# Optimization experiments

Measured on AMD Instinct MI355X. Metric: run time of the kernel, lower is better.

The kernel has to match this reference:

```python
import jax, jax.numpy as jnp
import numpy as np

L, H, DK = 4, 8, 64
NEG = -1e9
PAD = -9999.0


def _ln(z, g, b, eps=1e-6):
    # LayerNormalization: uses unbiased std (torch default) and divides by (std + eps)
    m = jnp.mean(z, axis=-1, keepdims=True)
    s = jnp.std(z, axis=-1, keepdims=True, ddof=1)
    return g * (z - m) / (s + eps) + b


def _mha(q_in, kv_in, w, bw, pw, pb, lnp, mask):
    B, Sq, D = q_in.shape
    q = (q_in @ w[0] + bw[0]).reshape(B, Sq, H, DK).transpose(0, 2, 1, 3)
    k = (kv_in @ w[1] + bw[1]).reshape(B, -1, H, DK).transpose(0, 2, 1, 3)
    v = (kv_in @ w[2] + bw[2]).reshape(B, -1, H, DK).transpose(0, 2, 1, 3)
    scores = jnp.einsum('bhqd,bhkd->bhqk', q, k) * (1.0 / np.sqrt(DK))
    if mask is not None:
        scores = jnp.where(mask[:, None, :, :], NEG, scores)
    attn = jax.nn.softmax(scores, axis=-1)
    ctx = jnp.einsum('bhqk,bhkd->bhqd', attn, v).transpose(0, 2, 1, 3).reshape(B, Sq, H * DK)
    return _ln(q_in + ctx @ pw + pb, lnp[0], lnp[1])


def _ffn(x, w1, b1, w2, b2, lnp):
    # kernel-1 conv1d == pointwise linear; w1:[d_ff,d_model], w2:[d_model,d_ff]
    h = jax.nn.relu(jnp.einsum('bsd,fd->bsf', x, w1) + b1)
    o = jnp.einsum('bsf,df->bsd', h, w2) + b2
    return _ln(x + o, lnp[0], lnp[1])


def _forward(enc_inputs, dec_inputs, emb_w, emb_b, pos_table,
             e_qkv_w, e_qkv_b, e_pw, e_pb, e_ln1, e_w1, e_b1, e_w2, e_b2, e_ln2,
             ds_qkv_w, ds_qkv_b, ds_pw, ds_pb, d_ln1,
             dc_qkv_w, dc_qkv_b, dc_pw, dc_pb, d_ln2,
             d_w1, d_b1, d_w2, d_b2, d_ln3):
    B, Se, F = enc_inputs.shape
    Sd = dec_inputs.shape[1]
    # ConvEmbeddingLayer: kernel-1 conv producing (d_model - n_features) channels, concat with raw inputs
    enc = jnp.concatenate([enc_inputs, jnp.einsum('bsf,of->bso', enc_inputs, emb_w) + emb_b], axis=-1)
    dec = jnp.concatenate([dec_inputs, jnp.einsum('bsf,of->bso', dec_inputs, emb_w) + emb_b], axis=-1)
    # PosEncoding with full lengths -> rows 1..S of the padded table
    enc = enc + pos_table[1:Se + 1]
    dec = dec + pos_table[1:Sd + 1]
    # masks per get_attn_pad_mask / get_attn_subsequent_mask
    enc_pad = jnp.sum(enc_inputs, axis=-1) <= PAD  # [B,Se]
    dec_pad = jnp.sum(dec_inputs, axis=-1) <= PAD  # [B,Sd]
    enc_mask = jnp.broadcast_to(enc_pad[:, None, :], (B, Se, Se))
    causal = jnp.triu(jnp.ones((Sd, Sd), dtype=bool), 1)
    dec_self_mask = jnp.broadcast_to(dec_pad[:, None, :], (B, Sd, Sd)) | causal
    cross_mask = jnp.broadcast_to(enc_pad[:, None, :], (B, Sd, Se))
    for i in range(L):
        enc = _mha(enc, enc, e_qkv_w[i], e_qkv_b[i], e_pw[i], e_pb[i], e_ln1[i], enc_mask)
        enc = _ffn(enc, e_w1[i], e_b1[i], e_w2[i], e_b2[i], e_ln2[i])
    for i in range(L):
        dec = _mha(dec, dec, ds_qkv_w[i], ds_qkv_b[i], ds_pw[i], ds_pb[i], d_ln1[i], dec_self_mask)
        dec = _mha(dec, enc, dc_qkv_w[i], dc_qkv_b[i], dc_pw[i], dc_pb[i], d_ln2[i], cross_mask)
        dec = _ffn(dec, d_w1[i], d_b1[i], d_w2[i], d_b2[i], d_ln3[i])
    return dec


def setup_inputs() -> dict:
    B, Se, Sd, F, Dm, Dff = 8, 512, 512, 32, 512, 2048
    key = jax.random.key(0)
    ks = iter(jax.random.split(key, 32))
    s = 0.02

    def n(shape, sc=s):
        return jax.random.normal(next(ks), shape, jnp.float32) * sc

    # sinusoidal PosEncoding table with leading pad row
    pos = np.arange(Se, dtype=np.float64)[:, None]
    j = np.arange(Dm)[None, :]
    ang = pos / np.power(10000.0, 2.0 * (j // 2) / Dm)
    ang[:, 0::2] = np.sin(ang[:, 0::2])
    ang[:, 1::2] = np.cos(ang[:, 1::2])
    pos_table = jnp.asarray(np.concatenate([np.zeros((1, Dm)), ang]).astype(np.float32))

    ln = jnp.broadcast_to(jnp.stack([jnp.ones(Dm), jnp.zeros(Dm)]), (L, 2, Dm)).astype(jnp.float32) + 0.0
    return {
        'enc_inputs': jax.random.normal(next(ks), (B, Se, F), jnp.float32),
        'dec_inputs': jax.random.normal(next(ks), (B, Sd, F), jnp.float32),
        'emb_w': n((Dm - F, F)), 'emb_b': jnp.zeros(Dm - F, jnp.float32),
        'pos_table': pos_table,
        'e_qkv_w': n((L, 3, Dm, H * DK)), 'e_qkv_b': jnp.zeros((L, 3, H * DK), jnp.float32),
        'e_pw': n((L, H * DK, Dm)), 'e_pb': jnp.zeros((L, Dm), jnp.float32), 'e_ln1': ln,
        'e_w1': n((L, Dff, Dm)), 'e_b1': jnp.zeros((L, Dff), jnp.float32),
        'e_w2': n((L, Dm, Dff)), 'e_b2': jnp.zeros((L, Dm), jnp.float32), 'e_ln2': ln,
        'ds_qkv_w': n((L, 3, Dm, H * DK)), 'ds_qkv_b': jnp.zeros((L, 3, H * DK), jnp.float32),
        'ds_pw': n((L, H * DK, Dm)), 'ds_pb': jnp.zeros((L, Dm), jnp.float32), 'd_ln1': ln,
        'dc_qkv_w': n((L, 3, Dm, H * DK)), 'dc_qkv_b': jnp.zeros((L, 3, H * DK), jnp.float32),
        'dc_pw': n((L, H * DK, Dm)), 'dc_pb': jnp.zeros((L, Dm), jnp.float32), 'd_ln2': ln,
        'd_w1': n((L, Dff, Dm)), 'd_b1': jnp.zeros((L, Dff), jnp.float32),
        'd_w2': n((L, Dm, Dff)), 'd_b2': jnp.zeros((L, Dm), jnp.float32), 'd_ln3': ln,
    }


def reference(enc_inputs, dec_inputs, emb_w, emb_b, pos_table,
              e_qkv_w, e_qkv_b, e_pw, e_pb, e_ln1, e_w1, e_b1, e_w2, e_b2, e_ln2,
              ds_qkv_w, ds_qkv_b, ds_pw, ds_pb, d_ln1,
              dc_qkv_w, dc_qkv_b, dc_pw, dc_pb, d_ln2,
              d_w1, d_b1, d_w2, d_b2, d_ln3):
    return _forward(enc_inputs, dec_inputs, emb_w, emb_b, pos_table,
                    e_qkv_w, e_qkv_b, e_pw, e_pb, e_ln1, e_w1, e_b1, e_w2, e_b2, e_ln2,
                    ds_qkv_w, ds_qkv_b, ds_pw, ds_pb, d_ln1,
                    dc_qkv_w, dc_qkv_b, dc_pw, dc_pb, d_ln2,
                    d_w1, d_b1, d_w2, d_b2, d_ln3)
```

## Files before the change

kernel.cpp:

```cpp
#include <hip/hip_runtime.h>
#include <cstdint>
#include <cstddef>

typedef unsigned short u16;
typedef __bf16 bf16x8 __attribute__((ext_vector_type(8)));
typedef float f32x4 __attribute__((ext_vector_type(4)));

constexpr int Bz = 8, Sq = 512, Hh = 8, DKd = 64, Dm = 512, Dff = 2048, NL = 4;
constexpr int TOK = Bz * Sq;
constexpr size_t MAT = (size_t)512 * 512;
constexpr size_t EL  = (size_t)TOK * Dm;

__device__ __forceinline__ float bf2f(u16 u) {
  union { uint32_t i; float f; } v; v.i = (uint32_t)u << 16; return v.f;
}
__device__ __forceinline__ u16 f2bf(float f) {
  union { float f; uint32_t i; } v; v.f = f;
  uint32_t i = v.i;
  i += 0x7fffu + ((i >> 16) & 1u);
  return (u16)(i >> 16);
}

__device__ __forceinline__ void gload16(const u16* g, u16* l) {
  __builtin_amdgcn_global_load_lds(
      (const __attribute__((address_space(1))) unsigned int*)g,
      (__attribute__((address_space(3))) unsigned int*)l, 16, 0, 0);
}

template<int BM, int BN>
__global__ __launch_bounds__(256)
void gemm_tile(const u16* __restrict__ A, const u16* __restrict__ Bt,
               const float* __restrict__ bias, u16* __restrict__ C,
               int K, int lda, long long sA, int ldb, long long sB,
               int ldc, long long sC, int cmode, int relu, int colofs)
{
  constexpr int HM = BM / 2, HN = BN / 2, MI = HM / 16, NI = HN / 16;
  __shared__ __align__(16) u16 As[BM * 32];
  __shared__ __align__(16) u16 Bs[BN * 32];
  const int bz = blockIdx.z;
  const u16* Ab = A + (size_t)bz * (size_t)sA + (size_t)(blockIdx.y * BM) * lda;
  const u16* Bb = Bt + (size_t)bz * (size_t)sB + (size_t)(blockIdx.x * BN) * ldb;
  const int tid  = threadIdx.x;
  const int lane = tid & 63;
  const int wid  = tid >> 6;
  const int l15  = lane & 15;
  const int quad = lane >> 4;
  const int wm   = wid >> 1, wn = wid & 1;

  f32x4 acc[MI][NI] = {};

  for (int k0 = 0; k0 < K; k0 += 32) {
#pragma unroll
    for (int i = 0; i < BM / 64; ++i) {
      const int s = tid + i * 256;
      const int c = (s & 3) ^ ((s >> 3) & 3);
      gload16(Ab + (size_t)(s >> 2) * lda + k0 + c * 8, As + s * 8);
    }
#pragma unroll
    for (int i = 0; i < BN / 64; ++i) {
      const int s = tid + i * 256;
      const int c = (s & 3) ^ ((s >> 3) & 3);
      gload16(Bb + (size_t)(s >> 2) * ldb + k0 + c * 8, Bs + s * 8);
    }
    __syncthreads();
    bf16x8 af[MI], bfr[NI];
#pragma unroll
    for (int mi = 0; mi < MI; ++mi) {
      const int ra = wm * HM + mi * 16 + l15;
      af[mi] = *(const bf16x8*)(As + ra * 32 + (quad ^ ((ra >> 1) & 3)) * 8);
    }
#pragma unroll
    for (int ni = 0; ni < NI; ++ni) {
      const int rb = wn * HN + ni * 16 + l15;
      bfr[ni] = *(const bf16x8*)(Bs + rb * 32 + (quad ^ ((rb >> 1) & 3)) * 8);
    }
#pragma unroll
    for (int mi = 0; mi < MI; ++mi)
#pragma unroll
      for (int ni = 0; ni < NI; ++ni)
        acc[mi][ni] = __builtin_amdgcn_mfma_f32_16x16x32_bf16(af[mi], bfr[ni], acc[mi][ni], 0, 0, 0);
    __syncthreads();
  }

  const int rblk = blockIdx.y * BM + wm * HM + quad * 4;
  const int cblk = blockIdx.x * BN + wn * HN;
#pragma unroll
  for (int ni = 0; ni < NI; ++ni) {
    const int col  = cblk + ni * 16 + l15;
    const int colx = colofs + col;
    const float bv = bias ? bias[colx] : 0.f;
#pragma unroll
    for (int mi = 0; mi < MI; ++mi) {
#pragma unroll
      for (int r = 0; r < 4; ++r) {
        float v = acc[mi][ni][r] + bv;
        if (relu) v = fmaxf(v, 0.f);
        const int grow = rblk + mi * 16 + r;
        size_t off;
        if (cmode == 0) {
          off = (size_t)bz * (size_t)sC + (size_t)grow * ldc + col;
        } else if (cmode == 3) {
          off = (size_t)(bz >> 3) * 262144 + (size_t)grow * 512 + (size_t)(bz & 7) * 64 + col;
        } else {
          const int sec = colx >> 9, n = colx & 511, h = n >> 6, d = n & 63;
          const int b = grow >> 9, s = grow & 511;
          if (sec == 0) v *= 0.125f;
          if (sec < 2) off = (size_t)sec * EL + (size_t)b * 262144 + (size_t)h * 32768 + (size_t)s * 64 + d;
          else         off = 2 * EL + (size_t)b * 262144 + (size_t)h * 32768 + (size_t)d * 512 + s;
        }
        C[off] = f2bf(v);
      }
    }
  }
}

__global__ __launch_bounds__(256)
void flash_attn(const u16* __restrict__ q, const u16* __restrict__ k,
                const u16* __restrict__ v, const unsigned char* __restrict__ pad,
                u16* __restrict__ ctx, int mtype)
{
  __shared__ __align__(16) u16 KVs[8192];
  __shared__ __align__(16) u16 Pw[4][2048];
  const int bh = blockIdx.y, b = bh >> 3, h = bh & 7;
  const int qt = blockIdx.x;
  const int tid = threadIdx.x, lane = tid & 63, wid = tid >> 6;
  const int l15 = lane & 15, quad = lane >> 4;
  const size_t bho = (size_t)bh * 32768;
  const int qrow = qt * 64 + wid * 16 + l15;
  const int qcd  = qt * 64 + wid * 16 + quad * 4;

  unsigned char* Ps = (unsigned char*)&Pw[0][0];
  if (tid < 128) ((uchar4*)Ps)[tid] = ((const uchar4*)(pad + b * 512))[tid];

  bf16x8 aq0 = *(const bf16x8*)(q + bho + (size_t)qrow * 64 + quad * 8);
  bf16x8 aq1 = *(const bf16x8*)(q + bho + (size_t)qrow * 64 + 32 + quad * 8);

  f32x4 S[32];
#pragma unroll
  for (int kc = 0; kc < 4; ++kc) {
    __syncthreads();
#pragma unroll
    for (int i = 0; i < 4; ++i) {
      const int s = tid + i * 256;
      const int row = s >> 3, c = (s & 7) ^ (row & 7);
      gload16(k + bho + (size_t)(kc * 128 + row) * 64 + c * 8, KVs + s * 8);
    }
    __syncthreads();
#pragma unroll
    for (int t = 0; t < 8; ++t) {
      const int sw = l15 & 7;
      bf16x8 b0 = *(const bf16x8*)(KVs + (t * 16 + l15) * 64 + (quad ^ sw) * 8);
      bf16x8 b1 = *(const bf16x8*)(KVs + (t * 16 + l15) * 64 + ((4 + quad) ^ sw) * 8);
      f32x4 z = {0.f, 0.f, 0.f, 0.f};
      z = __builtin_amdgcn_mfma_f32_16x16x32_bf16(aq0, b0, z, 0, 0, 0);
      S[kc * 8 + t] = __builtin_amdgcn_mfma_f32_16x16x32_bf16(aq1, b1, z, 0, 0, 0);
    }
  }

  unsigned pm = 0u;
#pragma unroll
  for (int t = 0; t < 32; ++t) pm |= (unsigned)(Ps[t * 16 + l15] != 0) << t;

  float inv[4];
#pragma unroll
  for (int r = 0; r < 4; ++r) {
    const int qg = qcd + r;
    float mx = -3.0e38f;
#pragma unroll
    for (int t = 0; t < 32; ++t) {
      const int col = t * 16 + l15;
      const bool m = ((pm >> t) & 1u) || (mtype == 1 && col > qg);
      const float val = m ? -1e9f : S[t][r];
      S[t][r] = val;
      mx = fmaxf(mx, val);
    }
#pragma unroll
    for (int o = 8; o > 0; o >>= 1) mx = fmaxf(mx, __shfl_xor(mx, o));
    float sm = 0.f;
#pragma unroll
    for (int t = 0; t < 32; ++t) { const float e = __expf(S[t][r] - mx); S[t][r] = e; sm += e; }
#pragma unroll
    for (int o = 8; o > 0; o >>= 1) sm += __shfl_xor(sm, o);
    inv[r] = 1.f / sm;
  }

  f32x4 O[4] = {};
  u16* myP = &Pw[wid][0];
#pragma unroll
  for (int kc = 0; kc < 4; ++kc) {
    __syncthreads();
#pragma unroll
    for (int i = 0; i < 4; ++i) {
      const int s = tid + i * 256;
      const int row = s >> 4, c = (s & 15) ^ (row & 15);
      gload16(v + bho + (size_t)row * 512 + kc * 128 + c * 8, KVs + s * 8);
    }
#pragma unroll
    for (int t = 0; t < 8; ++t)
#pragma unroll
      for (int r = 0; r < 4; ++r) {
        const int rowq = quad * 4 + r;
        const int c = 2 * t + (l15 >> 3);
        myP[rowq * 128 + (c ^ rowq) * 8 + (l15 & 7)] = f2bf(S[kc * 8 + t][r] * inv[r]);
      }
    __syncthreads();
#pragma unroll
    for (int kk = 0; kk < 4; ++kk) {
      bf16x8 ap = *(const bf16x8*)(myP + l15 * 128 + ((kk * 4 + quad) ^ l15) * 8);
#pragma unroll
      for (int ni = 0; ni < 4; ++ni) {
        bf16x8 bv = *(const bf16x8*)(KVs + (ni * 16 + l15) * 128 + ((kk * 4 + quad) ^ l15) * 8);
        O[ni] = __builtin_amdgcn_mfma_f32_16x16x32_bf16(ap, bv, O[ni], 0, 0, 0);
      }
    }
  }

  const int token = b * 512 + qcd;
#pragma unroll
  for (int ni = 0; ni < 4; ++ni)
#pragma unroll
    for (int r = 0; r < 4; ++r)
      ctx[(size_t)(token + r) * 512 + h * 64 + ni * 16 + l15] = f2bf(O[ni][r]);
}

__global__ __launch_bounds__(256)
void transpose512(const float* __restrict__ in, u16* __restrict__ out)
{
  __shared__ float tile[32][33];
  const size_t base = (size_t)blockIdx.z * MAT;
  int x = blockIdx.x * 32 + threadIdx.x;
  int y = blockIdx.y * 32 + threadIdx.y;
#pragma unroll
  for (int i = 0; i < 32; i += 8)
    tile[threadIdx.y + i][threadIdx.x] = in[base + (size_t)(y + i) * 512 + x];
  __syncthreads();
  x = blockIdx.y * 32 + threadIdx.x;
  y = blockIdx.x * 32 + threadIdx.y;
#pragma unroll
  for (int i = 0; i < 32; i += 8)
    out[base + (size_t)(y + i) * 512 + x] = f2bf(tile[threadIdx.x][threadIdx.y + i]);
}

__global__ __launch_bounds__(256)
void convert2(const float* __restrict__ w1, const float* __restrict__ w2,
              u16* __restrict__ o1, u16* __restrict__ o2, int n)
{
  int i = (blockIdx.x * 256 + threadIdx.x) * 4;
  if (i < n) {
    float4 a = *(const float4*)(w1 + i);
    float4 b = *(const float4*)(w2 + i);
    ushort4 ua = { f2bf(a.x), f2bf(a.y), f2bf(a.z), f2bf(a.w) };
    ushort4 ub = { f2bf(b.x), f2bf(b.y), f2bf(b.z), f2bf(b.w) };
    *(ushort4*)(o1 + i) = ua;
    *(ushort4*)(o2 + i) = ub;
  }
}

__global__ __launch_bounds__(256)
void embed_k(const float* __restrict__ x, const float* __restrict__ ew,
             const float* __restrict__ eb, const float* __restrict__ pos,
             u16* __restrict__ out)
{
  const int rs = blockIdx.x;
  const int s  = rs & 511;
  __shared__ float xr[32];
  const int t = threadIdx.x;
  if (t < 32) xr[t] = x[(size_t)rs * 32 + t];
  __syncthreads();
#pragma unroll
  for (int rep = 0; rep < 2; ++rep) {
    const int c = t + rep * 256;
    float v;
    if (c < 32) {
      v = xr[c];
    } else {
      const float* w = ew + (size_t)(c - 32) * 32;
      float acc = eb[c - 32];
#pragma unroll
      for (int f = 0; f < 32; ++f) acc += xr[f] * w[f];
      v = acc;
    }
    v += pos[(size_t)(s + 1) * 512 + c];
    out[(size_t)rs * 512 + c] = f2bf(v);
  }
}

__global__ __launch_bounds__(256)
void pad_k(const float* __restrict__ x, unsigned char* __restrict__ pad)
{
  int r = blockIdx.x * 256 + threadIdx.x;
  if (r < TOK) {
    float s = 0.f;
    for (int f = 0; f < 32; ++f) s += x[(size_t)r * 32 + f];
    pad[r] = (s <= -9999.f) ? 1 : 0;
  }
}

__global__ __launch_bounds__(256)
void add_ln(const u16* __restrict__ x, const u16* __restrict__ y,
            const float* __restrict__ g, const float* __restrict__ bb,
            u16* __restrict__ out)
{
  const int row  = blockIdx.x * 4 + (threadIdx.x >> 6);
  const int lane = threadIdx.x & 63;
  const int c0 = lane * 8;
  const size_t base = (size_t)row * Dm + c0;

  uint4 xr = *(const uint4*)(x + base);
  uint4 yr = *(const uint4*)(y + base);
  const u16* xh = (const u16*)&xr;
  const u16* yh = (const u16*)&yr;
  float z[8];
  float s = 0.f;
#pragma unroll
  for (int j = 0; j < 8; ++j) { z[j] = bf2f(xh[j]) + bf2f(yh[j]); s += z[j]; }
#pragma unroll
  for (int off = 32; off > 0; off >>= 1) s += __shfl_xor(s, off);
  const float mean = s * (1.f / 512.f);
  float ss = 0.f;
#pragma unroll
  for (int j = 0; j < 8; ++j) { z[j] -= mean; ss += z[j] * z[j]; }
#pragma unroll
  for (int off = 32; off > 0; off >>= 1) ss += __shfl_xor(ss, off);
  const float stdv = sqrtf(ss * (1.f / 511.f));
  const float inv = 1.f / (stdv + 1e-6f);

  float4 g0 = *(const float4*)(g + c0),  g1 = *(const float4*)(g + c0 + 4);
  float4 b0 = *(const float4*)(bb + c0), b1 = *(const float4*)(bb + c0 + 4);
  float gv[8] = { g0.x, g0.y, g0.z, g0.w, g1.x, g1.y, g1.z, g1.w };
  float bv[8] = { b0.x, b0.y, b0.z, b0.w, b1.x, b1.y, b1.z, b1.w };
  uint4 ow;
  u16* oh = (u16*)&ow;
#pragma unroll
  for (int j = 0; j < 8; ++j) oh[j] = f2bf(gv[j] * z[j] * inv + bv[j]);
  *(uint4*)(out + base) = ow;
}

__global__ __launch_bounds__(256)
void store_f32(const u16* __restrict__ in, float* __restrict__ out, int n)
{
  int i = (blockIdx.x * 256 + threadIdx.x) * 8;
  if (i < n) {
    uint4 raw = *(const uint4*)(in + i);
    const u16* h = (const u16*)&raw;
    float4 o0 = { bf2f(h[0]), bf2f(h[1]), bf2f(h[2]), bf2f(h[3]) };
    float4 o1 = { bf2f(h[4]), bf2f(h[5]), bf2f(h[6]), bf2f(h[7]) };
    *(float4*)(out + i) = o0;
    *(float4*)(out + i + 4) = o1;
  }
}

extern "C" void kernel_launch(void* const* d_in, const int* in_sizes, int n_in,
                              void* d_out, int out_size, void* d_ws, size_t ws_size,
                              hipStream_t stream)
{
  (void)in_sizes; (void)n_in; (void)out_size;
  const float* enc_in   = (const float*)d_in[0];
  const float* dec_in   = (const float*)d_in[1];
  const float* emb_w    = (const float*)d_in[2];
  const float* emb_b    = (const float*)d_in[3];
  const float* pos      = (const float*)d_in[4];
  const float* e_qkv_w  = (const float*)d_in[5];
  const float* e_qkv_b  = (const float*)d_in[6];
  const float* e_pw     = (const float*)d_in[7];
  const float* e_pb     = (const float*)d_in[8];
  const float* e_ln1    = (const float*)d_in[9];
  const float* e_w1     = (const float*)d_in[10];
  const float* e_b1     = (const float*)d_in[11];
  const float* e_w2     = (const float*)d_in[12];
  const float* e_b2     = (const float*)d_in[13];
  const float* e_ln2    = (const float*)d_in[14];
  const float* ds_qkv_w = (const float*)d_in[15];
  const float* ds_qkv_b = (const float*)d_in[16];
  const float* ds_pw    = (const float*)d_in[17];
  const float* ds_pb    = (const float*)d_in[18];
  const float* d_ln1    = (const float*)d_in[19];
  const float* dc_qkv_w = (const float*)d_in[20];
  const float* dc_qkv_b = (const float*)d_in[21];
  const float* dc_pw    = (const float*)d_in[22];
  const float* dc_pb    = (const float*)d_in[23];
  const float* d_ln2    = (const float*)d_in[24];
  const float* d_w1     = (const float*)d_in[25];
  const float* d_b1     = (const float*)d_in[26];
  const float* d_w2     = (const float*)d_in[27];
  const float* d_b2     = (const float*)d_in[28];
  const float* d_ln3    = (const float*)d_in[29];

  u16* ws  = (u16*)d_ws;
  u16* enc = ws;
  u16* dec = ws + EL;
  u16* qb  = ws + 2 * EL;
  u16* kb  = ws + 3 * EL;
  u16* vT  = ws + 4 * EL;
  u16* ctx = ws + 5 * EL;
  u16* t1  = ws + 6 * EL;
  u16* hff = ws + 7 * EL;
  u16* wf1 = ws + 11 * EL;
  u16* wf2 = ws + 11 * EL + EL / 2;
  u16* wT  = ws + 15 * EL;
  unsigned char* padE = (unsigned char*)(ws + 21 * EL);
  unsigned char* padD = padE + TOK;
  if (ws_size < 21 * EL * 2 + 2 * TOK) return;

  dim3 tb(32, 8);
  transpose512<<<dim3(16, 16, 12), tb, 0, stream>>>(e_qkv_w,  wT);
  transpose512<<<dim3(16, 16, 12), tb, 0, stream>>>(ds_qkv_w, wT + 12 * MAT);
  transpose512<<<dim3(16, 16, 12), tb, 0, stream>>>(dc_qkv_w, wT + 24 * MAT);
  transpose512<<<dim3(16, 16, 4),  tb, 0, stream>>>(e_pw,     wT + 36 * MAT);
  transpose512<<<dim3(16, 16, 4),  tb, 0, stream>>>(ds_pw,    wT + 40 * MAT);
  transpose512<<<dim3(16, 16, 4),  tb, 0, stream>>>(dc_pw,    wT + 44 * MAT);

  embed_k<<<TOK, 256, 0, stream>>>(enc_in, emb_w, emb_b, pos, enc);
  embed_k<<<TOK, 256, 0, stream>>>(dec_in, emb_w, emb_b, pos, dec);
  pad_k<<<TOK / 256, 256, 0, stream>>>(enc_in, padE);
  pad_k<<<TOK / 256, 256, 0, stream>>>(dec_in, padD);

  auto attention = [&](const u16* qsrc, const u16* kvsrc, const u16* wq3, const float* b3,
                       const u16* pwT, const float* pb, const float* ln,
                       const unsigned char* pad, int mtype, u16* x) {
    if (qsrc == kvsrc) {
      gemm_tile<64, 128><<<dim3(12, 64, 1), 256, 0, stream>>>(
          qsrc, wq3, b3, qb, 512, 512, 0, 512, 0, 0, 0, 4, 0, 0);
    } else {
      gemm_tile<64, 64><<<dim3(8, 64, 1), 256, 0, stream>>>(
          qsrc, wq3, b3, qb, 512, 512, 0, 512, 0, 0, 0, 4, 0, 0);
      gemm_tile<64, 128><<<dim3(8, 64, 1), 256, 0, stream>>>(
          kvsrc, wq3 + MAT, b3, qb, 512, 512, 0, 512, 0, 0, 0, 4, 0, 512);
    }
    flash_attn<<<dim3(8, 64), 256, 0, stream>>>(qb, kb, vT, pad, ctx, mtype);
    gemm_tile<64, 64><<<dim3(8, 64, 1), 256, 0, stream>>>(
        ctx, pwT, pb, t1, 512, 512, 0, 512, 0, 512, 0, 0, 0, 0);
    add_ln<<<TOK / 4, 256, 0, stream>>>(x, t1, ln, ln + 512, x);
  };

  auto ffn = [&](u16* x, const float* w1, const float* b1, const float* w2,
                 const float* b2, const float* ln) {
    convert2<<<1024, 256, 0, stream>>>(w1, w2, wf1, wf2, Dff * Dm);
    gemm_tile<128, 128><<<dim3(16, 32, 1), 256, 0, stream>>>(
        x, wf1, b1, hff, 512, 512, 0, 512, 0, 2048, 0, 0, 1, 0);
    gemm_tile<64, 64><<<dim3(8, 64, 1), 256, 0, stream>>>(
        hff, wf2, b2, t1, 2048, 2048, 0, 2048, 0, 512, 0, 0, 0, 0);
    add_ln<<<TOK / 4, 256, 0, stream>>>(x, t1, ln, ln + 512, x);
  };

  for (int i = 0; i < NL; ++i) {
    attention(enc, enc, wT + (size_t)(i * 3) * MAT, e_qkv_b + i * 3 * 512,
              wT + (size_t)(36 + i) * MAT, e_pb + i * 512, e_ln1 + i * 1024, padE, 0, enc);
    ffn(enc, e_w1 + (size_t)i * Dff * Dm, e_b1 + i * Dff,
        e_w2 + (size_t)i * Dm * Dff, e_b2 + i * Dm, e_ln2 + i * 1024);
  }

  for (int i = 0; i < NL; ++i) {
    attention(dec, dec, wT + (size_t)(12 + i * 3) * MAT, ds_qkv_b + i * 3 * 512,
              wT + (size_t)(40 + i) * MAT, ds_pb + i * 512, d_ln1 + i * 1024, padD, 1, dec);
    attention(dec, enc, wT + (size_t)(24 + i * 3) * MAT, dc_qkv_b + i * 3 * 512,
              wT + (size_t)(44 + i) * MAT, dc_pb + i * 512, d_ln2 + i * 1024, padE, 2, dec);
    ffn(dec, d_w1 + (size_t)i * Dff * Dm, d_b1 + i * Dff,
        d_w2 + (size_t)i * Dm * Dff, d_b2 + i * Dm, d_ln3 + i * 1024);
  }

  store_f32<<<(int)(EL / 8 / 256), 256, 0, stream>>>(dec, (float*)d_out, (int)EL);
}
```

Baseline: 1.489 ms.

## Widen GEMM K-step to 64, merge cross-attn QKV launch, batch weight prep kernels

The GEMM now stages 64-wide K slices in shared memory with an 8-way XOR swizzle and does two MFMA sub-steps per barrier pair, which halves the number of barriers and loads per K. Cross-attention's separate Q and KV projection launches become one launch that switches the A source by block column. The six transpose launches become one, the per-layer FFN weight conversions become a single upfront convert of all weights, and the padding-mask computation moves into the embedding kernel. The trade-off is double the shared memory per GEMM block, which may lower occupancy, and a larger workspace.

```diff
diff --git a/kernel.cpp b/kernel.cpp
--- a/kernel.cpp
+++ b/kernel.cpp
@@ -10,6 +10,7 @@
 constexpr int TOK = Bz * Sq;
 constexpr size_t MAT = (size_t)512 * 512;
 constexpr size_t EL  = (size_t)TOK * Dm;
+constexpr size_t WFT = (size_t)Dff * Dm;
 
 __device__ __forceinline__ float bf2f(u16 u) {
   union { uint32_t i; float f; } v; v.i = (uint32_t)u << 16; return v.f;
@@ -32,14 +33,23 @@
 void gemm_tile(const u16* __restrict__ A, const u16* __restrict__ Bt,
                const float* __restrict__ bias, u16* __restrict__ C,
                int K, int lda, long long sA, int ldb, long long sB,
-               int ldc, long long sC, int cmode, int relu, int colofs)
+               int ldc, long long sC, int cmode, int relu, int colofs,
+               const u16* A2, int xsplit)
 {
   constexpr int HM = BM / 2, HN = BN / 2, MI = HM / 16, NI = HN / 16;
-  __shared__ __align__(16) u16 As[BM * 32];
-  __shared__ __align__(16) u16 Bs[BN * 32];
+  __shared__ __align__(16) u16 As[BM * 64];
+  __shared__ __align__(16) u16 Bs[BN * 64];
   const int bz = blockIdx.z;
-  const u16* Ab = A + (size_t)bz * (size_t)sA + (size_t)(blockIdx.y * BM) * lda;
-  const u16* Bb = Bt + (size_t)bz * (size_t)sB + (size_t)(blockIdx.x * BN) * ldb;
+  const u16* Abase = A;
+  int colbase;
+  if (A2 && (int)blockIdx.x >= xsplit) {
+    Abase = A2;
+    colbase = 512 + ((int)blockIdx.x - xsplit) * BN;
+  } else {
+    colbase = colofs + (int)blockIdx.x * BN;
+  }
+  const u16* Ab = Abase + (size_t)bz * (size_t)sA + (size_t)(blockIdx.y * BM) * lda;
+  const u16* Bb = Bt + (size_t)bz * (size_t)sB + (size_t)colbase * ldb;
   const int tid  = threadIdx.x;
   const int lane = tid & 63;
   const int wid  = tid >> 6;
@@ -49,45 +59,46 @@
 
   f32x4 acc[MI][NI] = {};
 
-  for (int k0 = 0; k0 < K; k0 += 32) {
-#pragma unroll
-    for (int i = 0; i < BM / 64; ++i) {
+  for (int k0 = 0; k0 < K; k0 += 64) {
+#pragma unroll
+    for (int i = 0; i < BM / 32; ++i) {
       const int s = tid + i * 256;
-      const int c = (s & 3) ^ ((s >> 3) & 3);
-      gload16(Ab + (size_t)(s >> 2) * lda + k0 + c * 8, As + s * 8);
-    }
-#pragma unroll
-    for (int i = 0; i < BN / 64; ++i) {
+      const int row = s >> 3, c = (s & 7) ^ (row & 7);
+      gload16(Ab + (size_t)row * lda + k0 + c * 8, As + s * 8);
+    }
+#pragma unroll
+    for (int i = 0; i < BN / 32; ++i) {
       const int s = tid + i * 256;
-      const int c = (s & 3) ^ ((s >> 3) & 3);
-      gload16(Bb + (size_t)(s >> 2) * ldb + k0 + c * 8, Bs + s * 8);
-    }
-    __syncthreads();
-    bf16x8 af[MI], bfr[NI];
-#pragma unroll
-    for (int mi = 0; mi < MI; ++mi) {
-      const int ra = wm * HM + mi * 16 + l15;
-      af[mi] = *(const bf16x8*)(As + ra * 32 + (quad ^ ((ra >> 1) & 3)) * 8);
-    }
-#pragma unroll
-    for (int ni = 0; ni < NI; ++ni) {
-      const int rb = wn * HN + ni * 16 + l15;
-      bfr[ni] = *(const bf16x8*)(Bs + rb * 32 + (quad ^ ((rb >> 1) & 3)) * 8);
-    }
-#pragma unroll
-    for (int mi = 0; mi < MI; ++mi)
-#pragma unroll
-      for (int ni = 0; ni < NI; ++ni)
-        acc[mi][ni] = __builtin_amdgcn_mfma_f32_16x16x32_bf16(af[mi], bfr[ni], acc[mi][ni], 0, 0, 0);
+      const int row = s >> 3, c = (s & 7) ^ (row & 7);
+      gload16(Bb + (size_t)row * ldb + k0 + c * 8, Bs + s * 8);
+    }
+    __syncthreads();
+#pragma unroll
+    for (int kk = 0; kk < 2; ++kk) {
+      bf16x8 af[MI], bfr[NI];
+#pragma unroll
+      for (int mi = 0; mi < MI; ++mi) {
+        const int ra = wm * HM + mi * 16 + l15;
+        af[mi] = *(const bf16x8*)(As + ra * 64 + (((kk * 4 + quad) ^ (ra & 7))) * 8);
+      }
+#pragma unroll
+      for (int ni = 0; ni < NI; ++ni) {
+        const int rb = wn * HN + ni * 16 + l15;
+        bfr[ni] = *(const bf16x8*)(Bs + rb * 64 + (((kk * 4 + quad) ^ (rb & 7))) * 8);
+      }
+#pragma unroll
+      for (int mi = 0; mi < MI; ++mi)
+#pragma unroll
+        for (int ni = 0; ni < NI; ++ni)
+          acc[mi][ni] = __builtin_amdgcn_mfma_f32_16x16x32_bf16(af[mi], bfr[ni], acc[mi][ni], 0, 0, 0);
+    }
     __syncthreads();
   }
 
   const int rblk = blockIdx.y * BM + wm * HM + quad * 4;
-  const int cblk = blockIdx.x * BN + wn * HN;
 #pragma unroll
   for (int ni = 0; ni < NI; ++ni) {
-    const int col  = cblk + ni * 16 + l15;
-    const int colx = colofs + col;
+    const int colx = colbase + wn * HN + ni * 16 + l15;
     const float bv = bias ? bias[colx] : 0.f;
 #pragma unroll
     for (int mi = 0; mi < MI; ++mi) {
@@ -98,9 +109,7 @@
         const int grow = rblk + mi * 16 + r;
         size_t off;
         if (cmode == 0) {
-          off = (size_t)bz * (size_t)sC + (size_t)grow * ldc + col;
-        } else if (cmode == 3) {
-          off = (size_t)(bz >> 3) * 262144 + (size_t)grow * 512 + (size_t)(bz & 7) * 64 + col;
+          off = (size_t)bz * (size_t)sC + (size_t)grow * ldc + colx;
         } else {
           const int sec = colx >> 9, n = colx & 511, h = n >> 6, d = n & 63;
           const int b = grow >> 9, s = grow & 511;
@@ -224,42 +233,55 @@
 }
 
 __global__ __launch_bounds__(256)
-void transpose512(const float* __restrict__ in, u16* __restrict__ out)
+void transpose_all(const float* __restrict__ s0, const float* __restrict__ s1,
+                   const float* __restrict__ s2, const float* __restrict__ s3,
+                   const float* __restrict__ s4, const float* __restrict__ s5,
+                   u16* __restrict__ out)
 {
   __shared__ float tile[32][33];
-  const size_t base = (size_t)blockIdx.z * MAT;
+  const int z = blockIdx.z;
+  const float* src; int zi;
+  if      (z < 12) { src = s0; zi = z; }
+  else if (z < 24) { src = s1; zi = z - 12; }
+  else if (z < 36) { src = s2; zi = z - 24; }
+  else if (z < 40) { src = s3; zi = z - 36; }
+  else if (z < 44) { src = s4; zi = z - 40; }
+  else             { src = s5; zi = z - 44; }
+  const float* in = src + (size_t)zi * MAT;
+  u16* o = out + (size_t)z * MAT;
   int x = blockIdx.x * 32 + threadIdx.x;
   int y = blockIdx.y * 32 + threadIdx.y;
 #pragma unroll
   for (int i = 0; i < 32; i += 8)
-    tile[threadIdx.y + i][threadIdx.x] = in[base + (size_t)(y + i) * 512 + x];
+    tile[threadIdx.y + i][threadIdx.x] = in[(size_t)(y + i) * 512 + x];
   __syncthreads();
   x = blockIdx.y * 32 + threadIdx.x;
   y = blockIdx.x * 32 + threadIdx.y;
 #pragma unroll
   for (int i = 0; i < 32; i += 8)
-    out[base + (size_t)(y + i) * 512 + x] = f2bf(tile[threadIdx.x][threadIdx.y + i]);
-}
-
-__global__ __launch_bounds__(256)
-void convert2(const float* __restrict__ w1, const float* __restrict__ w2,
-              u16* __restrict__ o1, u16* __restrict__ o2, int n)
-{
+    o[(size_t)(y + i) * 512 + x] = f2bf(tile[threadIdx.x][threadIdx.y + i]);
+}
+
+__global__ __launch_bounds__(256)
+void convert4(const float* __restrict__ a, const float* __restrict__ b,
+              const float* __restrict__ c, const float* __restrict__ d,
+              u16* __restrict__ out, int n)
+{
+  const float* srcs[4] = { a, b, c, d };
+  const float* src = srcs[blockIdx.y];
+  u16* dst = out + (size_t)blockIdx.y * n;
   int i = (blockIdx.x * 256 + threadIdx.x) * 4;
   if (i < n) {
-    float4 a = *(const float4*)(w1 + i);
-    float4 b = *(const float4*)(w2 + i);
-    ushort4 ua = { f2bf(a.x), f2bf(a.y), f2bf(a.z), f2bf(a.w) };
-    ushort4 ub = { f2bf(b.x), f2bf(b.y), f2bf(b.z), f2bf(b.w) };
-    *(ushort4*)(o1 + i) = ua;
-    *(ushort4*)(o2 + i) = ub;
+    float4 v = *(const float4*)(src + i);
+    ushort4 u = { f2bf(v.x), f2bf(v.y), f2bf(v.z), f2bf(v.w) };
+    *(ushort4*)(dst + i) = u;
   }
 }
 
 __global__ __launch_bounds__(256)
 void embed_k(const float* __restrict__ x, const float* __restrict__ ew,
              const float* __restrict__ eb, const float* __restrict__ pos,
-             u16* __restrict__ out)
+             u16* __restrict__ out, unsigned char* __restrict__ padv)
 {
   const int rs = blockIdx.x;
   const int s  = rs & 511;
@@ -267,6 +289,12 @@
   const int t = threadIdx.x;
   if (t < 32) xr[t] = x[(size_t)rs * 32 + t];
   __syncthreads();
+  if (t == 0) {
+    float sacc = 0.f;
+#pragma unroll
+    for (int f = 0; f < 32; ++f) sacc += xr[f];
+    padv[rs] = (sacc <= -9999.f) ? 1 : 0;
+  }
 #pragma unroll
   for (int rep = 0; rep < 2; ++rep) {
     const int c = t + rep * 256;
@@ -282,17 +310,6 @@
     }
     v += pos[(size_t)(s + 1) * 512 + c];
     out[(size_t)rs * 512 + c] = f2bf(v);
-  }
-}
-
-__global__ __launch_bounds__(256)
-void pad_k(const float* __restrict__ x, unsigned char* __restrict__ pad)
-{
-  int r = blockIdx.x * 256 + threadIdx.x;
-  if (r < TOK) {
-    float s = 0.f;
-    for (int f = 0; f < 32; ++f) s += x[(size_t)r * 32 + f];
-    pad[r] = (s <= -9999.f) ? 1 : 0;
   }
 }
 
@@ -395,59 +412,48 @@
   u16* ctx = ws + 5 * EL;
   u16* t1  = ws + 6 * EL;
   u16* hff = ws + 7 * EL;
-  u16* wf1 = ws + 11 * EL;
-  u16* wf2 = ws + 11 * EL + EL / 2;
   u16* wT  = ws + 15 * EL;
   unsigned char* padE = (unsigned char*)(ws + 21 * EL);
   unsigned char* padD = padE + TOK;
-  if (ws_size < 21 * EL * 2 + 2 * TOK) return;
-
-  dim3 tb(32, 8);
-  transpose512<<<dim3(16, 16, 12), tb, 0, stream>>>(e_qkv_w,  wT);
-  transpose512<<<dim3(16, 16, 12), tb, 0, stream>>>(ds_qkv_w, wT + 12 * MAT);
-  transpose512<<<dim3(16, 16, 12), tb, 0, stream>>>(dc_qkv_w, wT + 24 * MAT);
-  transpose512<<<dim3(16, 16, 4),  tb, 0, stream>>>(e_pw,     wT + 36 * MAT);
-  transpose512<<<dim3(16, 16, 4),  tb, 0, stream>>>(ds_pw,    wT + 40 * MAT);
-  transpose512<<<dim3(16, 16, 4),  tb, 0, stream>>>(dc_pw,    wT + 44 * MAT);
-
-  embed_k<<<TOK, 256, 0, stream>>>(enc_in, emb_w, emb_b, pos, enc);
-  embed_k<<<TOK, 256, 0, stream>>>(dec_in, emb_w, emb_b, pos, dec);
-  pad_k<<<TOK / 256, 256, 0, stream>>>(enc_in, padE);
-  pad_k<<<TOK / 256, 256, 0, stream>>>(dec_in, padD);
+  u16* wfAll = ws + 22 * EL;
+  if (ws_size < 30 * EL * 2 + 2 * TOK) return;
+
+  transpose_all<<<dim3(16, 16, 48), dim3(32, 8), 0, stream>>>(
+      e_qkv_w, ds_qkv_w, dc_qkv_w, e_pw, ds_pw, dc_pw, wT);
+  convert4<<<dim3(4096, 4), 256, 0, stream>>>(e_w1, e_w2, d_w1, d_w2, wfAll, (int)(4 * WFT));
+  embed_k<<<TOK, 256, 0, stream>>>(enc_in, emb_w, emb_b, pos, enc, padE);
+  embed_k<<<TOK, 256, 0, stream>>>(dec_in, emb_w, emb_b, pos, dec, padD);
 
   auto attention = [&](const u16* qsrc, const u16* kvsrc, const u16* wq3, const float* b3,
                        const u16* pwT, const float* pb, const float* ln,
                        const unsigned char* pad, int mtype, u16* x) {
     if (qsrc == kvsrc) {
       gemm_tile<64, 128><<<dim3(12, 64, 1), 256, 0, stream>>>(
-          qsrc, wq3, b3, qb, 512, 512, 0, 512, 0, 0, 0, 4, 0, 0);
+          qsrc, wq3, b3, qb, 512, 512, 0, 512, 0, 0, 0, 4, 0, 0, nullptr, 0);
     } else {
-      gemm_tile<64, 64><<<dim3(8, 64, 1), 256, 0, stream>>>(
-          qsrc, wq3, b3, qb, 512, 512, 0, 512, 0, 0, 0, 4, 0, 0);
-      gemm_tile<64, 128><<<dim3(8, 64, 1), 256, 0, stream>>>(
-          kvsrc, wq3 + MAT, b3, qb, 512, 512, 0, 512, 0, 0, 0, 4, 0, 512);
+      gemm_tile<64, 128><<<dim3(12, 64, 1), 256, 0, stream>>>(
+          qsrc, wq3, b3, qb, 512, 512, 0, 512, 0, 0, 0, 4, 0, 0, kvsrc, 4);
     }
     flash_attn<<<dim3(8, 64), 256, 0, stream>>>(qb, kb, vT, pad, ctx, mtype);
     gemm_tile<64, 64><<<dim3(8, 64, 1), 256, 0, stream>>>(
-        ctx, pwT, pb, t1, 512, 512, 0, 512, 0, 512, 0, 0, 0, 0);
+        ctx, pwT, pb, t1, 512, 512, 0, 512, 0, 512, 0, 0, 0, 0, nullptr, 0);
     add_ln<<<TOK / 4, 256, 0, stream>>>(x, t1, ln, ln + 512, x);
   };
 
-  auto ffn = [&](u16* x, const float* w1, const float* b1, const float* w2,
+  auto ffn = [&](u16* x, const u16* w1b, const float* b1, const u16* w2b,
                  const float* b2, const float* ln) {
-    convert2<<<1024, 256, 0, stream>>>(w1, w2, wf1, wf2, Dff * Dm);
     gemm_tile<128, 128><<<dim3(16, 32, 1), 256, 0, stream>>>(
-        x, wf1, b1, hff, 512, 512, 0, 512, 0, 2048, 0, 0, 1, 0);
+        x, w1b, b1, hff, 512, 512, 0, 512, 0, 2048, 0, 0, 1, 0, nullptr, 0);
     gemm_tile<64, 64><<<dim3(8, 64, 1), 256, 0, stream>>>(
-        hff, wf2, b2, t1, 2048, 2048, 0, 2048, 0, 512, 0, 0, 0, 0);
+        hff, w2b, b2, t1, 2048, 2048, 0, 2048, 0, 512, 0, 0, 0, 0, nullptr, 0);
     add_ln<<<TOK / 4, 256, 0, stream>>>(x, t1, ln, ln + 512, x);
   };
 
   for (int i = 0; i < NL; ++i) {
     attention(enc, enc, wT + (size_t)(i * 3) * MAT, e_qkv_b + i * 3 * 512,
               wT + (size_t)(36 + i) * MAT, e_pb + i * 512, e_ln1 + i * 1024, padE, 0, enc);
-    ffn(enc, e_w1 + (size_t)i * Dff * Dm, e_b1 + i * Dff,
-        e_w2 + (size_t)i * Dm * Dff, e_b2 + i * Dm, e_ln2 + i * 1024);
+    ffn(enc, wfAll + (size_t)i * WFT, e_b1 + i * Dff,
+        wfAll + 4 * WFT + (size_t)i * WFT, e_b2 + i * Dm, e_ln2 + i * 1024);
   }
 
   for (int i = 0; i < NL; ++i) {
@@ -455,8 +461,8 @@
               wT + (size_t)(40 + i) * MAT, ds_pb + i * 512, d_ln1 + i * 1024, padD, 1, dec);
     attention(dec, enc, wT + (size_t)(24 + i * 3) * MAT, dc_qkv_b + i * 3 * 512,
               wT + (size_t)(44 + i) * MAT, dc_pb + i * 512, d_ln2 + i * 1024, padE, 2, dec);
-    ffn(dec, d_w1 + (size_t)i * Dff * Dm, d_b1 + i * Dff,
-        d_w2 + (size_t)i * Dm * Dff, d_b2 + i * Dm, d_ln3 + i * 1024);
+    ffn(dec, wfAll + 8 * WFT + (size_t)i * WFT, d_b1 + i * Dff,
+        wfAll + 12 * WFT + (size_t)i * WFT, d_b2 + i * Dm, d_ln3 + i * 1024);
   }
 
   store_f32<<<(int)(EL / 8 / 256), 256, 0, stream>>>(dec, (float*)d_out, (int)EL);
```

Measured after the change: 1.299 ms. -12.8%, faster.
